# Kernel optimization log

Hardware: AMD Instinct MI355X
Metric: run time of the kernel (lower is better)

Reference implementation:

```python
import jax, jax.numpy as jnp
import numpy as np

PH, PW = 7, 7  # pool_height, pool_width


def _bin_ids(n, lo, hi, d, nbins):
    """Assign each coordinate in [0,n) to its ROI bin (or to the dump segment `nbins`).

    Bins replicate the TF code: bin k covers [lo+k*d, lo+(k+1)*d) for k < nbins-1,
    and the last bin covers [lo+(nbins-1)*d, hi). d == (hi-lo)//nbins (trunc div).
    """
    coords = jnp.arange(n, dtype=jnp.int32)
    inside = (coords >= lo) & (coords < hi)
    b = jnp.minimum((coords - lo) // jnp.maximum(d, 1), nbins - 1)
    b = jnp.where(d > 0, b, nbins - 1)  # degenerate d==0: only last bin is non-empty
    return jnp.where(inside, b, nbins).astype(jnp.int32)


def _one_roi(image, roi, ph, pw):
    # image: [X, Y, C]; roi = (minX, minY, maxX, maxY) int32
    X, Y, C = image.shape
    minX, minY, maxX, maxY = roi[0], roi[1], roi[2], roi[3]
    dx = (maxX - minX) // pw
    dy = (maxY - minY) // ph
    xb = _bin_ids(X, minX, maxX, dx, pw)   # [X]
    yb = _bin_ids(Y, minY, maxY, dy, ph)   # [Y]
    # max over x within each x-bin -> [pw, Y, C]  (dump segment pw dropped)
    px = jax.ops.segment_max(image, xb, num_segments=pw + 1)[:pw]
    # max over y within each y-bin -> [ph, pw, C]
    py = jax.ops.segment_max(jnp.swapaxes(px, 0, 1), yb, num_segments=ph + 1)[:ph]
    return py  # [ph, pw, C], rows indexed by h (y-bins), cols by w (x-bins)


def setup_inputs() -> dict:
    key = jax.random.key(0)
    kf, kx1, kw, ky1, kh = jax.random.split(key, 5)
    B, H, W, C, N = 8, 128, 128, 128, 128
    features = jax.random.normal(kf, (B, H, W, C), dtype=jnp.float32)
    # valid ROIs: min < max, side length >= 2*pool so every bin is non-empty
    x1 = jax.random.randint(kx1, (B, N), 0, H // 2)
    wdt = jax.random.randint(kw, (B, N), 2 * PW, H // 2)
    y1 = jax.random.randint(ky1, (B, N), 0, W // 2)
    hgt = jax.random.randint(kh, (B, N), 2 * PH, W // 2)
    rois = jnp.stack([x1, y1, x1 + wdt, y1 + hgt], axis=-1).astype(jnp.int32)
    return {"features": features, "rois": rois}


def reference(features, rois):
    # features: [B, X, Y, C], rois: [B, N, 4] -> [B, N, PH, PW, C]
    per_img = jax.vmap(lambda img, r: _one_roi(img, r, PH, PW), in_axes=(None, 0))
    return jax.vmap(per_img)(features, rois)
```

## Files before the change

kernel.cpp:

```cpp
#include <hip/hip_runtime.h>

#define PH 7
#define PW 7
#define BINS (PH * PW)

__global__ __launch_bounds__(64) void roi_maxpool_kernel(
    const float* __restrict__ feat,
    const int*   __restrict__ rois,
    float*       __restrict__ out,
    int X, int Y, int C, int N, int xcd_swizzle)
{
    const int id = blockIdx.x;
    int b, rest;
    if (xcd_swizzle) { b = id & 7; rest = id >> 3; }
    else             { b = id / (N * BINS); rest = id % (N * BINS); }
    const int n  = rest / BINS;
    const int hw = rest % BINS;
    const int w  = hw % PW;
    const int h  = hw / PW;

    const int4 roi = *reinterpret_cast<const int4*>(&rois[(b * N + n) * 4]);
    const int minX = roi.x, minY = roi.y, maxX = roi.z, maxY = roi.w;

    const int dx = (maxX - minX) / PW;
    const int dy = (maxY - minY) / PH;

    const int xs = minX + w * dx;
    const int xe = (w == PW - 1) ? maxX : (xs + dx);
    const int ys = minY + h * dy;
    const int ye = (h == PH - 1) ? maxY : (ys + dy);

    const int t  = threadIdx.x;
    const int pp = t >> 5;
    const int c0 = (t & 31) * 4;

    const int y0    = ys + pp;
    const int cntL  = (ye - y0 + 1) >> 1;
    const int ylast = y0 + 2 * (cntL - 1);
    const int cnt0  = (ye - ys + 1) >> 1;

    float4 m; m.x = m.y = m.z = m.w = -INFINITY;

    for (int xi = xs; xi < xe; xi += 2) {
        const int x1 = (xi + 1 < xe) ? (xi + 1) : (xe - 1);
        const float* r0 = feat + ((long)(b * X + xi) * Y) * C + c0;
        const float* r1 = feat + ((long)(b * X + x1) * Y) * C + c0;
        for (int j = 0; j < cnt0; j += 2) {
            int ya = y0 + 2 * j;
            int yb = ya + 2;
            ya = (ya < ylast) ? ya : ylast;
            yb = (yb < ylast) ? yb : ylast;
            const float4 v0 = *reinterpret_cast<const float4*>(r0 + (long)ya * C);
            const float4 v1 = *reinterpret_cast<const float4*>(r0 + (long)yb * C);
            const float4 v2 = *reinterpret_cast<const float4*>(r1 + (long)ya * C);
            const float4 v3 = *reinterpret_cast<const float4*>(r1 + (long)yb * C);
            m.x = fmaxf(fmaxf(m.x, fmaxf(v0.x, v1.x)), fmaxf(v2.x, v3.x));
            m.y = fmaxf(fmaxf(m.y, fmaxf(v0.y, v1.y)), fmaxf(v2.y, v3.y));
            m.z = fmaxf(fmaxf(m.z, fmaxf(v0.z, v1.z)), fmaxf(v2.z, v3.z));
            m.w = fmaxf(fmaxf(m.w, fmaxf(v0.w, v1.w)), fmaxf(v2.w, v3.w));
        }
    }

    m.x = fmaxf(m.x, __shfl_xor(m.x, 32));
    m.y = fmaxf(m.y, __shfl_xor(m.y, 32));
    m.z = fmaxf(m.z, __shfl_xor(m.z, 32));
    m.w = fmaxf(m.w, __shfl_xor(m.w, 32));

    if (t < 32) {
        const int oidx = (((b * N + n) * PH + h) * PW + w) * C + c0;
        *reinterpret_cast<float4*>(&out[oidx]) = m;
    }
}

extern "C" void kernel_launch(void* const* d_in, const int* in_sizes, int n_in,
                              void* d_out, int out_size, void* d_ws, size_t ws_size,
                              hipStream_t stream) {
    const float* feat = (const float*)d_in[0];
    const int*   rois = (const int*)d_in[1];
    float*       out  = (float*)d_out;

    const int X = 128, Y = 128, C = 128;
    const int B = in_sizes[0] / (X * Y * C);
    const int N = in_sizes[1] / (4 * B);

    const int swz = (B == 8) ? 1 : 0;
    dim3 grid(B * N * BINS);
    roi_maxpool_kernel<<<grid, 64, 0, stream>>>(feat, rois, out, X, Y, C, N, swz);
}
```

Baseline: 139.0 us.

## Pair mirrored bins per 128-thread block and strength-reduce the inner y loop

Each block now holds two wavefronts that handle bins q and 48-q, so there are 25 blocks per ROI instead of 49 single-wave blocks, which lowers block-scheduling overhead and evens out work per block. The middle bin 24 is computed twice by both waves, which is redundant but harmless. The inner y loop now walks pointer increments over a fixed trip count, with the last one or two rows handled by a clamped epilogue. This replaces the per-iteration clamps and 64-bit address math, at the cost of some duplicated reads in the epilogue.

```diff
diff --git a/kernel.cpp b/kernel.cpp
--- a/kernel.cpp
+++ b/kernel.cpp
@@ -2,9 +2,10 @@
 
 #define PH 7
 #define PW 7
-#define BINS (PH * PW)
+#define BINS  (PH * PW)
+#define PAIRS 25
 
-__global__ __launch_bounds__(64) void roi_maxpool_kernel(
+__global__ __launch_bounds__(128) void roi_maxpool_kernel(
     const float* __restrict__ feat,
     const int*   __restrict__ rois,
     float*       __restrict__ out,
@@ -13,11 +14,13 @@
     const int id = blockIdx.x;
     int b, rest;
     if (xcd_swizzle) { b = id & 7; rest = id >> 3; }
-    else             { b = id / (N * BINS); rest = id % (N * BINS); }
-    const int n  = rest / BINS;
-    const int hw = rest % BINS;
-    const int w  = hw % PW;
-    const int h  = hw / PW;
+    else             { b = id / (N * PAIRS); rest = id % (N * PAIRS); }
+    const int n  = rest / PAIRS;
+    const int q  = rest % PAIRS;
+    const int wv = threadIdx.x >> 6;
+    const int bin = wv ? (48 - q) : q;
+    const int w = bin % PW;
+    const int h = bin / PW;
 
     const int4 roi = *reinterpret_cast<const int4*>(&rois[(b * N + n) * 4]);
     const int minX = roi.x, minY = roi.y, maxX = roi.z, maxY = roi.w;
@@ -30,35 +33,47 @@
     const int ys = minY + h * dy;
     const int ye = (h == PH - 1) ? maxY : (ys + dy);
 
-    const int t  = threadIdx.x;
+    const int t  = threadIdx.x & 63;
     const int pp = t >> 5;
     const int c0 = (t & 31) * 4;
 
+    const int H     = ye - ys;
     const int y0    = ys + pp;
-    const int cntL  = (ye - y0 + 1) >> 1;
-    const int ylast = y0 + 2 * (cntL - 1);
-    const int cnt0  = (ye - ys + 1) >> 1;
+    const int cnt   = (H + 1 - pp) >> 1;
+    const int ylast = y0 + 2 * (cnt - 1);
+    const int trips = H >> 2;
+    const int yA    = (ylast - 2 > y0) ? (ylast - 2) : y0;
+    const int ea    = (yA - y0) * C;
+    const int eb    = (ylast - y0) * C;
 
     float4 m; m.x = m.y = m.z = m.w = -INFINITY;
 
+    const float* base = feat + b * X * Y * C + c0;
     for (int xi = xs; xi < xe; xi += 2) {
         const int x1 = (xi + 1 < xe) ? (xi + 1) : (xe - 1);
-        const float* r0 = feat + ((long)(b * X + xi) * Y) * C + c0;
-        const float* r1 = feat + ((long)(b * X + x1) * Y) * C + c0;
-        for (int j = 0; j < cnt0; j += 2) {
-            int ya = y0 + 2 * j;
-            int yb = ya + 2;
-            ya = (ya < ylast) ? ya : ylast;
-            yb = (yb < ylast) ? yb : ylast;
-            const float4 v0 = *reinterpret_cast<const float4*>(r0 + (long)ya * C);
-            const float4 v1 = *reinterpret_cast<const float4*>(r0 + (long)yb * C);
-            const float4 v2 = *reinterpret_cast<const float4*>(r1 + (long)ya * C);
-            const float4 v3 = *reinterpret_cast<const float4*>(r1 + (long)yb * C);
+        const float* r0 = base + (xi * Y + y0) * C;
+        const float* r1 = base + (x1 * Y + y0) * C;
+        const float* p0 = r0;
+        const float* p1 = r1;
+        for (int it = 0; it < trips; ++it) {
+            const float4 v0 = *reinterpret_cast<const float4*>(p0);
+            const float4 v1 = *reinterpret_cast<const float4*>(p0 + 2 * C);
+            const float4 v2 = *reinterpret_cast<const float4*>(p1);
+            const float4 v3 = *reinterpret_cast<const float4*>(p1 + 2 * C);
+            p0 += 4 * C; p1 += 4 * C;
             m.x = fmaxf(fmaxf(m.x, fmaxf(v0.x, v1.x)), fmaxf(v2.x, v3.x));
             m.y = fmaxf(fmaxf(m.y, fmaxf(v0.y, v1.y)), fmaxf(v2.y, v3.y));
             m.z = fmaxf(fmaxf(m.z, fmaxf(v0.z, v1.z)), fmaxf(v2.z, v3.z));
             m.w = fmaxf(fmaxf(m.w, fmaxf(v0.w, v1.w)), fmaxf(v2.w, v3.w));
         }
+        const float4 e0 = *reinterpret_cast<const float4*>(r0 + ea);
+        const float4 e1 = *reinterpret_cast<const float4*>(r0 + eb);
+        const float4 e2 = *reinterpret_cast<const float4*>(r1 + ea);
+        const float4 e3 = *reinterpret_cast<const float4*>(r1 + eb);
+        m.x = fmaxf(fmaxf(m.x, fmaxf(e0.x, e1.x)), fmaxf(e2.x, e3.x));
+        m.y = fmaxf(fmaxf(m.y, fmaxf(e0.y, e1.y)), fmaxf(e2.y, e3.y));
+        m.z = fmaxf(fmaxf(m.z, fmaxf(e0.z, e1.z)), fmaxf(e2.z, e3.z));
+        m.w = fmaxf(fmaxf(m.w, fmaxf(e0.w, e1.w)), fmaxf(e2.w, e3.w));
     }
 
     m.x = fmaxf(m.x, __shfl_xor(m.x, 32));
@@ -84,6 +99,6 @@
     const int N = in_sizes[1] / (4 * B);
 
     const int swz = (B == 8) ? 1 : 0;
-    dim3 grid(B * N * BINS);
-    roi_maxpool_kernel<<<grid, 64, 0, stream>>>(feat, rois, out, X, Y, C, N, swz);
+    dim3 grid(B * N * PAIRS);
+    roi_maxpool_kernel<<<grid, 128, 0, stream>>>(feat, rois, out, X, Y, C, N, swz);
 }
```

New measurement: 139.0 us. About the same (+0.0%).
